# Optimization experiments

Measured on AMD Instinct MI355X. Metric: run time of the kernel, lower is better.

## Reference

```python
import jax, jax.numpy as jnp
import numpy as np


def setup_inputs() -> dict:
    key = jax.random.key(0)
    k1, k2, k3, k4, k5 = jax.random.split(key, 5)
    n_obs, m_test, k_pts, d = 192, 64, 32, 8
    return {
        "X_obs": jax.random.normal(k1, (n_obs, k_pts, d), dtype=jnp.float32),
        "A_obs": 0.1 * jax.random.normal(k2, (n_obs, k_pts), dtype=jnp.float32),
        "X_test": jax.random.normal(k3, (m_test, k_pts, d), dtype=jnp.float32),
        "A_test": 0.1 * jax.random.normal(k4, (m_test, k_pts), dtype=jnp.float32),
        "ys": jax.random.normal(k5, (n_obs,), dtype=jnp.float32),
        "rho_base": jnp.ones((d,), dtype=jnp.float32),   # base-kernel per-dim lengthscales
        "rho": jnp.float32(1.0),                          # function-kernel lengthscale^2
        "g": jnp.float32(1e-3),                           # nugget
        "nu": jnp.float32(1.0),                           # signal variance
        "b": jnp.float32(0.0),                            # prior mean
    }


def _function_kernel(X, A, rho_base, rho):
    # X: [N, k, d] support points, A: [N, k] coefficients.
    # Base SE kernel between all support points of all functions.
    N, k, d = X.shape
    Z = (X / rho_base).reshape(N * k, d)
    sq = jnp.sum(Z * Z, axis=-1)
    sqd = jnp.maximum(sq[:, None] + sq[None, :] - 2.0 * (Z @ Z.T), 0.0)  # [Nk, Nk]
    Kbase = jnp.exp(-0.5 * sqd)
    # Quadratic forms C[i,j] = a_i^T K(X_i, X_j) a_j (fused over all pairs,
    # replacing the original per-pair python double loop).
    T = Kbase.reshape(N, k, N, k)
    C = jnp.einsum('ip,ipjq,jq->ij', A, T, A)  # [N, N]
    q = jnp.diag(C)                            # per-function RKHS norms^2 (cached once)
    D2 = jnp.maximum(q[:, None] + q[None, :] - 2.0 * C, 0.0)  # squared RKHS distances
    # profile(d / sqrt(rho)) with SE profile => exp(-0.5 * d^2 / rho)
    return jnp.exp(-0.5 * D2 / rho)


def reference(X_obs, A_obs, X_test, A_test, ys, rho_base, rho, g, nu, b):
    n = X_obs.shape[0]
    X = jnp.concatenate([X_obs, X_test], axis=0)
    A = jnp.concatenate([A_obs, A_test], axis=0)
    Kf = _function_kernel(X, A, rho_base, rho)  # [N, N]
    Koo = nu * (Kf[:n, :n] + g * jnp.eye(n, dtype=Kf.dtype))
    Kox = nu * Kf[:n, n:]   # [n, m]
    Kxx = nu * Kf[n:, n:]   # [m, m]
    # gp_posterior
    gain = jnp.linalg.solve(Koo, Kox).T           # [m, n]
    mean = b + gain @ (ys - b)                    # [m]
    cov = Kxx - gain @ Kox                        # [m, m]
    Kbx = jnp.ones((1, n), dtype=Kf.dtype) @ gain.T  # [1, m]
    cov = cov + (1.0 - Kbx).T @ (1.0 - Kbx) / jnp.linalg.inv(Koo).sum()
    return mean, cov
```

## Files before the change

kernel.cpp:

```cpp
#include <hip/hip_runtime.h>
#include <math.h>

#define NOBS  192
#define MTEST 64
#define NF    256
#define KP    32
#define DD    8
#define NK    (NF*KP)
#define NB    32
#define NBLK  6
#define SB    69
#define PSTR  36
#define NTHR  768
#define NWAVE 12

__device__ __host__ __forceinline__ int PROF(int i) {
  int a = i >> 2, m = i & 3;
  return ((a + 1) * ((a << 1) + m)) << 2;
}

#define WS_Z   0
#define WS_A   (WS_Z + NK*DD)
#define WS_MH  (WS_A + NK)
#define WS_C   (WS_MH + NK)
#define WS_S   (WS_C + NF*NF)
#define WS_LP  (WS_S + NOBS*SB)
#define WS_BB  (WS_LP + 18816)

__global__ __launch_bounds__(256) void k0_prep(
    const float* __restrict__ Xo, const float* __restrict__ Ao,
    const float* __restrict__ Xt, const float* __restrict__ At,
    const float* __restrict__ rho_base, float* __restrict__ Z,
    float* __restrict__ Acat, float* __restrict__ MH) {
  int p = blockIdx.x * 256 + threadIdx.x;
  if (p >= NK) return;
  const float* xp = (p < NOBS * KP) ? (Xo + p * DD) : (Xt + (p - NOBS * KP) * DD);
  float4 x0 = *(const float4*)(xp);
  float4 x1 = *(const float4*)(xp + 4);
  float4 r0 = *(const float4*)(rho_base);
  float4 r1 = *(const float4*)(rho_base + 4);
  const float s = 1.2011224087864498f;
  float z0 = x0.x / r0.x * s, z1 = x0.y / r0.y * s, z2 = x0.z / r0.z * s, z3 = x0.w / r0.w * s;
  float z4 = x1.x / r1.x * s, z5 = x1.y / r1.y * s, z6 = x1.z / r1.z * s, z7 = x1.w / r1.w * s;
  float n = z0 * z0 + z1 * z1 + z2 * z2 + z3 * z3 + z4 * z4 + z5 * z5 + z6 * z6 + z7 * z7;
  *(float4*)(Z + p * DD) = make_float4(z0, z1, z2, z3);
  *(float4*)(Z + p * DD + 4) = make_float4(z4, z5, z6, z7);
  MH[p] = -0.5f * n;
  Acat[p] = (p < NOBS * KP) ? Ao[p] : At[p - NOBS * KP];
}

__global__ __launch_bounds__(256) void k1_C(
    const float* __restrict__ Z, const float* __restrict__ A,
    const float* __restrict__ MH, float* __restrict__ C) {
  int ti = blockIdx.x >> 5, tj = blockIdx.x & 31;
  if (tj < ti) return;
  __shared__ float Zi[8 * KP * DD];
  __shared__ float Ai[8 * KP];
  __shared__ float MHi[8 * KP];
  int t = threadIdx.x;
  {
    const float4* src = (const float4*)(Z + ti * (8 * KP * DD));
    ((float4*)Zi)[t * 2] = src[t * 2];
    ((float4*)Zi)[t * 2 + 1] = src[t * 2 + 1];
    Ai[t] = A[ti * (8 * KP) + t];
    MHi[t] = MH[ti * (8 * KP) + t];
  }
  int jl = t >> 5, q = t & 31;
  int jf = tj * 8 + jl;
  const float4* Zq = (const float4*)(Z + (jf * KP + q) * DD);
  float4 zq0 = Zq[0], zq1 = Zq[1];
  float aq = A[jf * KP + q];
  float mq = MH[jf * KP + q];
  __syncthreads();

  float acc[8];
#pragma unroll
  for (int ii = 0; ii < 8; ++ii) acc[ii] = 0.f;
#pragma unroll
  for (int ii = 0; ii < 8; ++ii) {
    float a_ = acc[ii];
#pragma unroll 8
    for (int p = 0; p < KP; ++p) {
      const float4* Zp = (const float4*)(Zi + (ii * KP + p) * DD);
      float4 zp0 = Zp[0], zp1 = Zp[1];
      float d = zp0.x * zq0.x;
      d = fmaf(zp0.y, zq0.y, d);
      d = fmaf(zp0.z, zq0.z, d);
      d = fmaf(zp0.w, zq0.w, d);
      d = fmaf(zp1.x, zq1.x, d);
      d = fmaf(zp1.y, zq1.y, d);
      d = fmaf(zp1.z, zq1.z, d);
      d = fmaf(zp1.w, zq1.w, d);
      float arg = d + MHi[ii * KP + p] + mq;
      float ex;
      asm("v_exp_f32 %0, %1" : "=v"(ex) : "v"(arg));
      a_ = fmaf(Ai[ii * KP + p], ex, a_);
    }
    acc[ii] = a_;
  }
#pragma unroll
  for (int ii = 0; ii < 8; ++ii) {
    float v = acc[ii] * aq;
#pragma unroll
    for (int off = 16; off > 0; off >>= 1) v += __shfl_xor(v, off, 64);
    if (q == 0) {
      int fi = ti * 8 + ii, fj = jf;
      C[fi * NF + fj] = v;
      C[fj * NF + fi] = v;
    }
  }
}

__global__ __launch_bounds__(256) void k2_build(
    const float* __restrict__ Cm, const float* __restrict__ ys,
    const float* __restrict__ pb, const float* __restrict__ prho,
    const float* __restrict__ pg, const float* __restrict__ pnu,
    float* __restrict__ Lbuf, float* __restrict__ Bbuf) {
  int i = blockIdx.x;
  int t = threadIdx.x;
  float nu = pnu[0];
  float c2 = -0.72134752044448f / prho[0];
  float gn = nu * pg[0];
  float qi = Cm[i * NF + i];
  int rowlen = (i & ~3) + 4;
  int base = PROF(i);
  for (int l = t; l < rowlen; l += 256) {
    float v = 0.f;
    if (l <= i) {
      float D2 = qi + Cm[l * NF + l] - 2.f * Cm[i * NF + l];
      D2 = D2 > 0.f ? D2 : 0.f;
      v = nu * exp2f(c2 * D2) + (l == i ? gn : 0.f);
    }
    Lbuf[base + l] = v;
  }
  if (t < SB) {
    float v;
    if (t < 64) {
      float D2 = qi + Cm[(NOBS + t) * NF + NOBS + t] - 2.f * Cm[i * NF + NOBS + t];
      D2 = D2 > 0.f ? D2 : 0.f;
      v = nu * exp2f(c2 * D2);
    } else if (t == 64) v = ys[i] - pb[0];
    else if (t == 65) v = 1.0f;
    else v = 0.f;
    Bbuf[i * SB + t] = v;
  }
}

__device__ __forceinline__ void phaseA(float* Lp, float* MiB, int kbA, int lane) {
  float row[32];
  int base = PROF(kbA + lane) + kbA;
#pragma unroll
  for (int c = 0; c < 32; c += 4) {
    float4 v = *(const float4*)&Lp[base + c];
    row[c] = v.x; row[c + 1] = v.y; row[c + 2] = v.z; row[c + 3] = v.w;
  }
#pragma unroll
  for (int j = 0; j < 32; ++j) {
    float dj = __shfl(row[j], j, 64);
    float rs = 1.0f / sqrtf(dj);
    float cl = row[j] * rs;
    row[j] = cl;
#pragma unroll
    for (int c = j + 1; c < 32; ++c)
      row[c] = fmaf(-cl, __shfl(cl, c, 64), row[c]);
  }
#pragma unroll
  for (int c = 0; c < 32; c += 4) {
    *(float4*)&MiB[lane * PSTR + c] =
        make_float4(row[c], row[c + 1], row[c + 2], row[c + 3]);
  }
  float x[32];
#pragma unroll
  for (int i2 = 0; i2 < 32; ++i2) {
    float vi = MiB[i2 * PSTR + lane];
    float acc = (i2 == lane) ? 1.0f : 0.0f;
#pragma unroll
    for (int k = 0; k < 32; ++k) {
      if (k < i2) acc = fmaf(-__shfl(vi, k, 64), x[k], acc);
    }
    x[i2] = acc / __shfl(vi, i2, 64);
  }
#pragma unroll
  for (int i2 = 0; i2 < 32; ++i2) MiB[i2 * PSTR + lane] = x[i2];
}

__global__ __launch_bounds__(NTHR, 3) void k3_factor_solve(
    const float* __restrict__ Lsrc, const float* __restrict__ Bsrc,
    float* __restrict__ Sout) {
  __shared__ float Lp[18816];
  __shared__ float Bm[NOBS * SB];
  __shared__ float Pn[160 * PSTR];
  __shared__ float Mi[2][32 * PSTR];

  int tid = threadIdx.x;
  int lane = tid & 63;
  int w = tid >> 6;

  for (int e = tid; e < 18816 / 4; e += NTHR)
    ((float4*)Lp)[e] = ((const float4*)Lsrc)[e];
  for (int e = tid; e < (NOBS * SB) / 4; e += NTHR)
    ((float4*)Bm)[e] = ((const float4*)Bsrc)[e];
  __syncthreads();

  if (w == 0 && lane < 32) phaseA(Lp, Mi[0], 0, lane);
  __syncthreads();

  for (int b = 0; b < NBLK; ++b) {
    int kb = b * NB;
    int rem = NOBS - kb - NB;
    const float* Mc = Mi[b & 1];

    float yv[5];
    if (rem > 0) {
      int c = tid & 31;
      int rg = tid >> 5;
      float Mreg[32];
#pragma unroll
      for (int qq = 0; qq < 32; qq += 4) {
        float4 v = *(const float4*)&Mc[c * PSTR + qq];
        Mreg[qq] = v.x; Mreg[qq + 1] = v.y; Mreg[qq + 2] = v.z; Mreg[qq + 3] = v.w;
      }
#pragma unroll 7
      for (int rr = 0; rr < 7; ++rr) {
        int r = rg + rr * 24;
        if (r < rem) {
          int abase = PROF(kb + NB + r) + kb;
          float a0 = 0.f, a1 = 0.f, a2 = 0.f, a3 = 0.f;
#pragma unroll
          for (int qq = 0; qq < 32; qq += 4) {
            float4 av = *(const float4*)&Lp[abase + qq];
            a0 = fmaf(av.x, Mreg[qq], a0);
            a1 = fmaf(av.y, Mreg[qq + 1], a1);
            a2 = fmaf(av.z, Mreg[qq + 2], a2);
            a3 = fmaf(av.w, Mreg[qq + 3], a3);
          }
          Pn[r * PSTR + c] = (a0 + a1) + (a2 + a3);
        }
      }
    }
    if (tid < 512) {
      int r2 = tid >> 4, cg = tid & 15;
      float Mrow[32];
#pragma unroll
      for (int qq = 0; qq < 32; qq += 4) {
        float4 v = *(const float4*)&Mc[r2 * PSTR + qq];
        Mrow[qq] = v.x; Mrow[qq + 1] = v.y; Mrow[qq + 2] = v.z; Mrow[qq + 3] = v.w;
      }
#pragma unroll 5
      for (int jj = 0; jj < 5; ++jj) {
        int col = cg + 16 * jj;
        float a0 = 0.f, a1 = 0.f, a2 = 0.f, a3 = 0.f;
        if (col < SB) {
#pragma unroll
          for (int k = 0; k < 32; k += 4) {
            a0 = fmaf(Mrow[k],     Bm[(kb + k) * SB + col], a0);
            a1 = fmaf(Mrow[k + 1], Bm[(kb + k + 1) * SB + col], a1);
            a2 = fmaf(Mrow[k + 2], Bm[(kb + k + 2) * SB + col], a2);
            a3 = fmaf(Mrow[k + 3], Bm[(kb + k + 3) * SB + col], a3);
          }
        }
        yv[jj] = (a0 + a1) + (a2 + a3);
      }
    }
    __syncthreads();

    if (tid < 512) {
      int r2 = tid >> 4, cg = tid & 15;
#pragma unroll 5
      for (int jj = 0; jj < 5; ++jj) {
        int col = cg + 16 * jj;
        if (col < SB) Bm[(kb + r2) * SB + col] = yv[jj];
      }
    }
    if (rem > 0) {
      for (int idx = tid; idx < 1024; idx += NTHR) {
        int r = idx >> 5, c = idx & 31;
        if (c <= r) {
          float a0 = 0.f, a1 = 0.f, a2 = 0.f, a3 = 0.f;
#pragma unroll
          for (int qq = 0; qq < 32; qq += 4) {
            float4 u = *(const float4*)&Pn[r * PSTR + qq];
            float4 vv = *(const float4*)&Pn[c * PSTR + qq];
            a0 = fmaf(u.x, vv.x, a0);
            a1 = fmaf(u.y, vv.y, a1);
            a2 = fmaf(u.z, vv.z, a2);
            a3 = fmaf(u.w, vv.w, a3);
          }
          Lp[PROF(kb + NB + r) + kb + NB + c] -= (a0 + a1) + (a2 + a3);
        }
      }
    }
    __syncthreads();

    if (rem > 0) {
      if (w == 0) {
        if (lane < 32) phaseA(Lp, Mi[(b + 1) & 1], kb + NB, lane);
      } else {
        int wp = w - 1;
        float yc[32], yc2[32];
        bool has2 = lane < 2;
        int colx = 64 + lane;
#pragma unroll
        for (int k = 0; k < 32; ++k) {
          yc[k] = Bm[(kb + k) * SB + lane];
          yc2[k] = has2 ? Bm[(kb + k) * SB + colx] : 0.f;
        }
        for (int rt = wp; rt < rem; rt += (NWAVE - 1)) {
          int gr = kb + NB + rt;
          float a0 = Bm[gr * SB + lane], a1 = 0.f;
          float b0 = has2 ? Bm[gr * SB + colx] : 0.f, b1 = 0.f;
#pragma unroll
          for (int k = 0; k < 32; k += 4) {
            float4 pv = *(const float4*)&Pn[rt * PSTR + k];
            a0 = fmaf(-pv.x, yc[k], a0);     b0 = fmaf(-pv.x, yc2[k], b0);
            a1 = fmaf(-pv.y, yc[k + 1], a1); b1 = fmaf(-pv.y, yc2[k + 1], b1);
            a0 = fmaf(-pv.z, yc[k + 2], a0); b0 = fmaf(-pv.z, yc2[k + 2], b0);
            a1 = fmaf(-pv.w, yc[k + 3], a1); b1 = fmaf(-pv.w, yc2[k + 3], b1);
          }
          Bm[gr * SB + lane] = a0 + a1;
          if (has2) Bm[gr * SB + colx] = b0 + b1;
        }
        for (int c0 = 0; c0 < rem; c0 += 64) {
          int cc = c0 + lane;
          int ccl = cc < 160 ? cc : 159;
          float Pc[32];
#pragma unroll
          for (int qq = 0; qq < 32; qq += 4) {
            float4 v = *(const float4*)&Pn[ccl * PSTR + qq];
            Pc[qq] = v.x; Pc[qq + 1] = v.y; Pc[qq + 2] = v.z; Pc[qq + 3] = v.w;
          }
          int rstart = c0 > 32 ? c0 : 32;
          for (int r = rstart + wp; r < rem; r += (NWAVE - 1)) {
            float a0 = 0.f, a1 = 0.f, a2 = 0.f, a3 = 0.f;
#pragma unroll
            for (int qq = 0; qq < 32; qq += 4) {
              float4 u = *(const float4*)&Pn[r * PSTR + qq];
              a0 = fmaf(u.x, Pc[qq], a0);
              a1 = fmaf(u.y, Pc[qq + 1], a1);
              a2 = fmaf(u.z, Pc[qq + 2], a2);
              a3 = fmaf(u.w, Pc[qq + 3], a3);
            }
            float tot = (a0 + a1) + (a2 + a3);
            if (cc <= r) {
              Lp[PROF(kb + NB + r) + kb + NB + cc] -= tot;
            }
          }
        }
      }
      __syncthreads();
    }
  }

  for (int e = tid; e < (NOBS * SB) / 4; e += NTHR)
    ((float4*)Sout)[e] = ((const float4*)Bm)[e];
}

__global__ __launch_bounds__(64) void k4_post(
    const float* __restrict__ S, const float* __restrict__ Cm,
    const float* __restrict__ pb, const float* __restrict__ prho,
    const float* __restrict__ pnu, float* __restrict__ out) {
  int a = blockIdx.x;
  int bb = threadIdx.x;
  float cv0 = 0.f, cv1 = 0.f, m0 = 0.f, m1 = 0.f;
  float ka0 = 0.f, ka1 = 0.f, kc0 = 0.f, kc1 = 0.f, d0 = 0.f, d1 = 0.f;
#pragma unroll 4
  for (int i = 0; i < NOBS; i += 2) {
    float sa0 = S[i * SB + a],        sb0 = S[i * SB + bb];
    float sy0 = S[i * SB + 64],       s10 = S[i * SB + 65];
    float sa1 = S[(i + 1) * SB + a],  sb1 = S[(i + 1) * SB + bb];
    float sy1 = S[(i + 1) * SB + 64], s11 = S[(i + 1) * SB + 65];
    cv0 = fmaf(sa0, sb0, cv0);  cv1 = fmaf(sa1, sb1, cv1);
    m0 = fmaf(sa0, sy0, m0);    m1 = fmaf(sa1, sy1, m1);
    ka0 = fmaf(sa0, s10, ka0);  ka1 = fmaf(sa1, s11, ka1);
    kc0 = fmaf(sb0, s10, kc0);  kc1 = fmaf(sb1, s11, kc1);
    d0 = fmaf(s10, s10, d0);    d1 = fmaf(s11, s11, d1);
  }
  float nu = pnu[0];
  float c2 = -0.72134752044448f / prho[0];
  float qa = Cm[(NOBS + a) * NF + NOBS + a];
  float qb = Cm[(NOBS + bb) * NF + NOBS + bb];
  float cab = Cm[(NOBS + a) * NF + NOBS + bb];
  float D2 = qa + qb - 2.f * cab;
  D2 = D2 > 0.f ? D2 : 0.f;
  float kxx = nu * exp2f(c2 * D2);
  float kbxa = 1.f - (ka0 + ka1);
  float kbxb = 1.f - (kc0 + kc1);
  float den = d0 + d1;
  out[MTEST + a * MTEST + bb] = kxx - (cv0 + cv1) + kbxa * kbxb / den;
  if (bb == 0) out[a] = pb[0] + (m0 + m1);
}

extern "C" void kernel_launch(void* const* d_in, const int* in_sizes, int n_in,
                              void* d_out, int out_size, void* d_ws, size_t ws_size,
                              hipStream_t stream) {
  const float* Xo = (const float*)d_in[0];
  const float* Ao = (const float*)d_in[1];
  const float* Xt = (const float*)d_in[2];
  const float* At = (const float*)d_in[3];
  const float* ys = (const float*)d_in[4];
  const float* rb = (const float*)d_in[5];
  const float* prho = (const float*)d_in[6];
  const float* pg = (const float*)d_in[7];
  const float* pnu = (const float*)d_in[8];
  const float* pb = (const float*)d_in[9];
  float* ws = (float*)d_ws;
  float* Z = ws + WS_Z;
  float* Acat = ws + WS_A;
  float* MH = ws + WS_MH;
  float* C = ws + WS_C;
  float* S = ws + WS_S;
  float* Lbuf = ws + WS_LP;
  float* Bbuf = ws + WS_BB;
  float* out = (float*)d_out;

  hipLaunchKernelGGL(k0_prep, dim3(NK / 256), dim3(256), 0, stream,
                     Xo, Ao, Xt, At, rb, Z, Acat, MH);
  hipLaunchKernelGGL(k1_C, dim3(1024), dim3(256), 0, stream, Z, Acat, MH, C);
  hipLaunchKernelGGL(k2_build, dim3(NOBS), dim3(256), 0, stream,
                     C, ys, pb, prho, pg, pnu, Lbuf, Bbuf);
  hipLaunchKernelGGL(k3_factor_solve, dim3(1), dim3(NTHR), 0, stream,
                     Lbuf, Bbuf, S);
  hipLaunchKernelGGL(k4_post, dim3(MTEST), dim3(MTEST), 0, stream, S, C, pb, prho, pnu, out);
}
```

Before: 276.0 us.

## Fuse prep into C kernel, launch only upper-triangle tiles, rework trailing B columns

Removes the separate prep kernel. Each C-tile block now scales X by the rho_base lengthscales, computes norms and gathers A on the fly, and the kernel launches only the 528 upper-triangular tile pairs instead of 1024 blocks with early exits. The single-block factor/solve kernel changes its occupancy hint to an amdgpu_waves_per_eu attribute. It also moves the two extra right-hand-side columns (64,65) out of the per-wave register arrays into a separate per-thread pass, cutting register pressure. The cost is recomputing the Z normalisation redundantly per tile and serial LDS reads in the new column pass.

```diff
diff --git a/kernel.cpp b/kernel.cpp
--- a/kernel.cpp
+++ b/kernel.cpp
@@ -6,7 +6,6 @@
 #define NF    256
 #define KP    32
 #define DD    8
-#define NK    (NF*KP)
 #define NB    32
 #define NBLK  6
 #define SB    69
@@ -19,60 +18,61 @@
   return ((a + 1) * ((a << 1) + m)) << 2;
 }
 
-#define WS_Z   0
-#define WS_A   (WS_Z + NK*DD)
-#define WS_MH  (WS_A + NK)
-#define WS_C   (WS_MH + NK)
+#define WS_C   0
 #define WS_S   (WS_C + NF*NF)
 #define WS_LP  (WS_S + NOBS*SB)
 #define WS_BB  (WS_LP + 18816)
 
-__global__ __launch_bounds__(256) void k0_prep(
+__global__ __launch_bounds__(256) void k1_C(
     const float* __restrict__ Xo, const float* __restrict__ Ao,
     const float* __restrict__ Xt, const float* __restrict__ At,
-    const float* __restrict__ rho_base, float* __restrict__ Z,
-    float* __restrict__ Acat, float* __restrict__ MH) {
-  int p = blockIdx.x * 256 + threadIdx.x;
-  if (p >= NK) return;
-  const float* xp = (p < NOBS * KP) ? (Xo + p * DD) : (Xt + (p - NOBS * KP) * DD);
-  float4 x0 = *(const float4*)(xp);
-  float4 x1 = *(const float4*)(xp + 4);
-  float4 r0 = *(const float4*)(rho_base);
-  float4 r1 = *(const float4*)(rho_base + 4);
-  const float s = 1.2011224087864498f;
-  float z0 = x0.x / r0.x * s, z1 = x0.y / r0.y * s, z2 = x0.z / r0.z * s, z3 = x0.w / r0.w * s;
-  float z4 = x1.x / r1.x * s, z5 = x1.y / r1.y * s, z6 = x1.z / r1.z * s, z7 = x1.w / r1.w * s;
-  float n = z0 * z0 + z1 * z1 + z2 * z2 + z3 * z3 + z4 * z4 + z5 * z5 + z6 * z6 + z7 * z7;
-  *(float4*)(Z + p * DD) = make_float4(z0, z1, z2, z3);
-  *(float4*)(Z + p * DD + 4) = make_float4(z4, z5, z6, z7);
-  MH[p] = -0.5f * n;
-  Acat[p] = (p < NOBS * KP) ? Ao[p] : At[p - NOBS * KP];
-}
-
-__global__ __launch_bounds__(256) void k1_C(
-    const float* __restrict__ Z, const float* __restrict__ A,
-    const float* __restrict__ MH, float* __restrict__ C) {
-  int ti = blockIdx.x >> 5, tj = blockIdx.x & 31;
-  if (tj < ti) return;
+    const float* __restrict__ rho_base, float* __restrict__ C) {
+  int tt = blockIdx.x;
+  int ti = 0, len = 32, rm = tt;
+  while (rm >= len) { rm -= len; ++ti; --len; }
+  int tj = ti + rm;
+
   __shared__ float Zi[8 * KP * DD];
   __shared__ float Ai[8 * KP];
   __shared__ float MHi[8 * KP];
-  int t = threadIdx.x;
+  int th = threadIdx.x;
+  const float s = 1.2011224087864498f;
+  float4 rr0 = *(const float4*)(rho_base);
+  float4 rr1 = *(const float4*)(rho_base + 4);
+  float i0 = s / rr0.x, i1 = s / rr0.y, i2 = s / rr0.z, i3 = s / rr0.w;
+  float i4 = s / rr1.x, i5 = s / rr1.y, i6 = s / rr1.z, i7 = s / rr1.w;
+
   {
-    const float4* src = (const float4*)(Z + ti * (8 * KP * DD));
-    ((float4*)Zi)[t * 2] = src[t * 2];
-    ((float4*)Zi)[t * 2 + 1] = src[t * 2 + 1];
-    Ai[t] = A[ti * (8 * KP) + t];
-    MHi[t] = MH[ti * (8 * KP) + t];
-  }
-  int jl = t >> 5, q = t & 31;
-  int jf = tj * 8 + jl;
-  const float4* Zq = (const float4*)(Z + (jf * KP + q) * DD);
-  float4 zq0 = Zq[0], zq1 = Zq[1];
-  float aq = A[jf * KP + q];
-  float mq = MH[jf * KP + q];
+    int gpi = ti * 256 + th;
+    const float* xp = (gpi < NOBS * KP) ? (Xo + gpi * DD) : (Xt + (gpi - NOBS * KP) * DD);
+    float4 x0 = *(const float4*)(xp);
+    float4 x1 = *(const float4*)(xp + 4);
+    float z0 = x0.x * i0, z1 = x0.y * i1, z2 = x0.z * i2, z3 = x0.w * i3;
+    float z4 = x1.x * i4, z5 = x1.y * i5, z6 = x1.z * i6, z7 = x1.w * i7;
+    float n = z0 * z0 + z1 * z1 + z2 * z2 + z3 * z3 +
+              z4 * z4 + z5 * z5 + z6 * z6 + z7 * z7;
+    *(float4*)&Zi[th * DD] = make_float4(z0, z1, z2, z3);
+    *(float4*)&Zi[th * DD + 4] = make_float4(z4, z5, z6, z7);
+    MHi[th] = -0.5f * n;
+    Ai[th] = (gpi < NOBS * KP) ? Ao[gpi] : At[gpi - NOBS * KP];
+  }
+  float4 zq0, zq1;
+  float aq, mq;
+  {
+    int gpj = tj * 256 + th;
+    const float* xp = (gpj < NOBS * KP) ? (Xo + gpj * DD) : (Xt + (gpj - NOBS * KP) * DD);
+    float4 x0 = *(const float4*)(xp);
+    float4 x1 = *(const float4*)(xp + 4);
+    zq0 = make_float4(x0.x * i0, x0.y * i1, x0.z * i2, x0.w * i3);
+    zq1 = make_float4(x1.x * i4, x1.y * i5, x1.z * i6, x1.w * i7);
+    float n = zq0.x * zq0.x + zq0.y * zq0.y + zq0.z * zq0.z + zq0.w * zq0.w +
+              zq1.x * zq1.x + zq1.y * zq1.y + zq1.z * zq1.z + zq1.w * zq1.w;
+    mq = -0.5f * n;
+    aq = (gpj < NOBS * KP) ? Ao[gpj] : At[gpj - NOBS * KP];
+  }
   __syncthreads();
 
+  int q = th & 31;
   float acc[8];
 #pragma unroll
   for (int ii = 0; ii < 8; ++ii) acc[ii] = 0.f;
@@ -104,7 +104,7 @@
 #pragma unroll
     for (int off = 16; off > 0; off >>= 1) v += __shfl_xor(v, off, 64);
     if (q == 0) {
-      int fi = ti * 8 + ii, fj = jf;
+      int fi = ti * 8 + ii, fj = tj * 8 + (th >> 5);
       C[fi * NF + fj] = v;
       C[fj * NF + fi] = v;
     }
@@ -184,7 +184,9 @@
   for (int i2 = 0; i2 < 32; ++i2) MiB[i2 * PSTR + lane] = x[i2];
 }
 
-__global__ __launch_bounds__(NTHR, 3) void k3_factor_solve(
+__global__ __launch_bounds__(NTHR)
+__attribute__((amdgpu_waves_per_eu(3, 3)))
+void k3_factor_solve(
     const float* __restrict__ Lsrc, const float* __restrict__ Bsrc,
     float* __restrict__ Sout) {
   __shared__ float Lp[18816];
@@ -297,28 +299,42 @@
         if (lane < 32) phaseA(Lp, Mi[(b + 1) & 1], kb + NB, lane);
       } else {
         int wp = w - 1;
-        float yc[32], yc2[32];
-        bool has2 = lane < 2;
-        int colx = 64 + lane;
-#pragma unroll
-        for (int k = 0; k < 32; ++k) {
-          yc[k] = Bm[(kb + k) * SB + lane];
-          yc2[k] = has2 ? Bm[(kb + k) * SB + colx] : 0.f;
-        }
+        float yc[32];
+#pragma unroll
+        for (int k = 0; k < 32; ++k) yc[k] = Bm[(kb + k) * SB + lane];
         for (int rt = wp; rt < rem; rt += (NWAVE - 1)) {
           int gr = kb + NB + rt;
           float a0 = Bm[gr * SB + lane], a1 = 0.f;
-          float b0 = has2 ? Bm[gr * SB + colx] : 0.f, b1 = 0.f;
 #pragma unroll
           for (int k = 0; k < 32; k += 4) {
             float4 pv = *(const float4*)&Pn[rt * PSTR + k];
-            a0 = fmaf(-pv.x, yc[k], a0);     b0 = fmaf(-pv.x, yc2[k], b0);
-            a1 = fmaf(-pv.y, yc[k + 1], a1); b1 = fmaf(-pv.y, yc2[k + 1], b1);
-            a0 = fmaf(-pv.z, yc[k + 2], a0); b0 = fmaf(-pv.z, yc2[k + 2], b0);
-            a1 = fmaf(-pv.w, yc[k + 3], a1); b1 = fmaf(-pv.w, yc2[k + 3], b1);
+            a0 = fmaf(-pv.x, yc[k], a0);
+            a1 = fmaf(-pv.y, yc[k + 1], a1);
+            a0 = fmaf(-pv.z, yc[k + 2], a0);
+            a1 = fmaf(-pv.w, yc[k + 3], a1);
           }
           Bm[gr * SB + lane] = a0 + a1;
-          if (has2) Bm[gr * SB + colx] = b0 + b1;
+        }
+        {
+          int r65 = tid - 64;
+          if (r65 < rem) {
+            int gr = kb + NB + r65;
+            float a64 = Bm[gr * SB + 64], a65 = Bm[gr * SB + 65];
+#pragma unroll
+            for (int qq = 0; qq < 32; qq += 4) {
+              float4 pv = *(const float4*)&Pn[r65 * PSTR + qq];
+              a64 = fmaf(-pv.x, Bm[(kb + qq) * SB + 64], a64);
+              a65 = fmaf(-pv.x, Bm[(kb + qq) * SB + 65], a65);
+              a64 = fmaf(-pv.y, Bm[(kb + qq + 1) * SB + 64], a64);
+              a65 = fmaf(-pv.y, Bm[(kb + qq + 1) * SB + 65], a65);
+              a64 = fmaf(-pv.z, Bm[(kb + qq + 2) * SB + 64], a64);
+              a65 = fmaf(-pv.z, Bm[(kb + qq + 2) * SB + 65], a65);
+              a64 = fmaf(-pv.w, Bm[(kb + qq + 3) * SB + 64], a64);
+              a65 = fmaf(-pv.w, Bm[(kb + qq + 3) * SB + 65], a65);
+            }
+            Bm[gr * SB + 64] = a64;
+            Bm[gr * SB + 65] = a65;
+          }
         }
         for (int c0 = 0; c0 < rem; c0 += 64) {
           int cc = c0 + lane;
@@ -404,18 +420,14 @@
   const float* pnu = (const float*)d_in[8];
   const float* pb = (const float*)d_in[9];
   float* ws = (float*)d_ws;
-  float* Z = ws + WS_Z;
-  float* Acat = ws + WS_A;
-  float* MH = ws + WS_MH;
   float* C = ws + WS_C;
   float* S = ws + WS_S;
   float* Lbuf = ws + WS_LP;
   float* Bbuf = ws + WS_BB;
   float* out = (float*)d_out;
 
-  hipLaunchKernelGGL(k0_prep, dim3(NK / 256), dim3(256), 0, stream,
-                     Xo, Ao, Xt, At, rb, Z, Acat, MH);
-  hipLaunchKernelGGL(k1_C, dim3(1024), dim3(256), 0, stream, Z, Acat, MH, C);
+  hipLaunchKernelGGL(k1_C, dim3(528), dim3(256), 0, stream,
+                     Xo, Ao, Xt, At, rb, C);
   hipLaunchKernelGGL(k2_build, dim3(NOBS), dim3(256), 0, stream,
                      C, ys, pb, prho, pg, pnu, Lbuf, Bbuf);
   hipLaunchKernelGGL(k3_factor_solve, dim3(1), dim3(NTHR), 0, stream,
```

Result: faster. 260.1 us (-5.8%).
